# Optimization experiments

Hardware: AMD Instinct MI355X
Metric: run time of the kernel (lower is better)

The kernel has to match this reference:

```python
import jax, jax.numpy as jnp
import numpy as np

N_STRING = 6
N_SCALAR = 20
D_MODEL = 256
TOP_K = 4
LN_EPS = 1e-5


def setup_inputs() -> dict:
    key = jax.random.key(0)
    ks = jax.random.split(key, 16)
    B, d = 32768, D_MODEL
    s = 0.02
    inp = {
        "string_strategy_encodings": jax.random.normal(ks[0], (B, N_STRING, d), jnp.float32),
        "scalar_strategy_encodings": jax.random.normal(ks[1], (B, N_SCALAR, d), jnp.float32),
        "pair_scores": jax.random.normal(ks[2], (N_STRING, N_SCALAR), jnp.float32) * 0.1,
        "score_temperature": jnp.asarray(1.0, jnp.float32),
        # cross_modal_mlp: Linear(3d, d) -> ReLU -> Linear(d, d)
        "cm_w1": jax.random.normal(ks[3], (3 * d, d), jnp.float32) * s,
        "cm_b1": jnp.zeros((d,), jnp.float32),
        "cm_w2": jax.random.normal(ks[4], (d, d), jnp.float32) * s,
        "cm_b2": jnp.zeros((d,), jnp.float32),
        # diff_mlp: Linear(2d, d) -> ReLU -> Linear(d, d)
        "df_w1": jax.random.normal(ks[5], (2 * d, d), jnp.float32) * s,
        "df_b1": jnp.zeros((d,), jnp.float32),
        "df_w2": jax.random.normal(ks[6], (d, d), jnp.float32) * s,
        "df_b2": jnp.zeros((d,), jnp.float32),
        # fusion_mlp: Linear(3d, 2d) -> ReLU -> Linear(2d, d)
        "fu_w1": jax.random.normal(ks[7], (3 * d, 2 * d), jnp.float32) * s,
        "fu_b1": jnp.zeros((2 * d,), jnp.float32),
        "fu_w2": jax.random.normal(ks[8], (2 * d, d), jnp.float32) * s,
        "fu_b2": jnp.zeros((d,), jnp.float32),
        # output LayerNorm
        "ln_g": jnp.ones((d,), jnp.float32),
        "ln_b": jnp.zeros((d,), jnp.float32),
    }
    return inp


def _layernorm(x, g, b):
    mu = jnp.mean(x, axis=-1, keepdims=True)
    var = jnp.mean(jnp.square(x - mu), axis=-1, keepdims=True)
    return (x - mu) * jax.lax.rsqrt(var + LN_EPS) * g + b


def reference(string_strategy_encodings, scalar_strategy_encodings, pair_scores,
              score_temperature, cm_w1, cm_b1, cm_w2, cm_b2,
              df_w1, df_b1, df_w2, df_b2, fu_w1, fu_b1, fu_w2, fu_b2, ln_g, ln_b):
    n_string = string_strategy_encodings.shape[1]
    scores = pair_scores[:n_string, :]  # (6, 20); no masks (None path)
    flat = scores.reshape(-1)
    topk_vals, topk_idx = jax.lax.top_k(flat, TOP_K)
    ti = topk_idx // N_SCALAR  # string strategy indices (K,)
    tj = topk_idx % N_SCALAR   # scalar strategy indices (K,)
    temp = jnp.maximum(score_temperature, 0.1)
    weights = jax.nn.softmax(topk_vals / temp)  # (K,)

    s = jnp.take(string_strategy_encodings, ti, axis=1)  # (B, K, d)
    c = jnp.take(scalar_strategy_encodings, tj, axis=1)  # (B, K, d)
    prod = s * c

    cross_in = jnp.concatenate([s, c, prod], axis=-1)  # (B, K, 3d)
    cross_f = jax.nn.relu(cross_in @ cm_w1 + cm_b1) @ cm_w2 + cm_b2

    diff = s - c
    diff_in = jnp.concatenate([diff, jnp.abs(diff)], axis=-1)  # (B, K, 2d)
    diff_f = jax.nn.relu(diff_in @ df_w1 + df_b1) @ df_w2 + df_b2

    combined = jnp.concatenate([cross_f, diff_f, prod], axis=-1)  # (B, K, 3d)
    fused = jax.nn.relu(combined @ fu_w1 + fu_b1) @ fu_w2 + fu_b2
    rel = _layernorm(fused, ln_g, ln_b)  # (B, K, d)

    return jnp.einsum('k,bkd->bd', weights, rel)
```

## Files before the change

### kernel.cpp

```cpp
#include <hip/hip_runtime.h>
#include <stdint.h>


typedef __attribute__((ext_vector_type(8))) short frag8;
typedef __attribute__((ext_vector_type(4))) float f4;
typedef __attribute__((ext_vector_type(4))) int   i4;

#define MFMA16(a,b,c) __builtin_amdgcn_mfma_f32_16x16x32_bf16((a),(b),(c),0,0,0)

__device__ __forceinline__ short f2bf(float x) {
  unsigned u = __float_as_uint(x);
  return (short)((u + 0x7FFFu + ((u >> 16) & 1u)) >> 16);
}
__device__ __forceinline__ float bf2f(short s) {
  return __uint_as_float(((unsigned)(unsigned short)s) << 16);
}
__device__ __forceinline__ frag8 ldg8(const short* __restrict__ p) {
  return *reinterpret_cast<const frag8*>(p);
}


__global__ __launch_bounds__(256) void k_prep(
    const float* __restrict__ ps, const float* __restrict__ tempp,
    const float* __restrict__ w1, const float* __restrict__ w2,
    const float* __restrict__ dw1, const float* __restrict__ dw2,
    const float* __restrict__ fw1, const float* __restrict__ fw2,
    short* __restrict__ w1p, short* __restrict__ w2p,
    short* __restrict__ dw1p, short* __restrict__ dw2p,
    short* __restrict__ fw1p, short* __restrict__ fw2p,
    float* __restrict__ hdrf, int* __restrict__ hdri)
{
  if (blockIdx.x == 0) {
    const int lane = threadIdx.x;
    if (lane < 64) {
      const float NEG = -3.4e38f;
      float v0 = (lane < 120)      ? ps[lane]      : NEG;
      float v1 = (lane + 64 < 120) ? ps[lane + 64] : NEG;
      const int i0 = lane, i1 = lane + 64;
      unsigned elim = 0;
      float tv[4]; int bi[4];
      #pragma unroll
      for (int t = 0; t < 4; ++t) {
        float c0 = (elim & 1u) ? NEG : v0;
        float c1 = (elim & 2u) ? NEG : v1;
        float cv; int ci;
        if (c1 > c0) { cv = c1; ci = i1; } else { cv = c0; ci = i0; }
        #pragma unroll
        for (int off = 32; off >= 1; off >>= 1) {
          float ov = __shfl_xor(cv, off, 64);
          int   oi = __shfl_xor(ci, off, 64);
          if (ov > cv || (ov == cv && oi < ci)) { cv = ov; ci = oi; }
        }
        tv[t] = cv; bi[t] = ci;
        if (ci == i0) elim |= 1u;
        if (ci == i1) elim |= 2u;
      }
      if (lane == 0) {
        float tmp = fmaxf(tempp[0], 0.1f);
        float mx = tv[0];
        float e[4], s = 0.f;
        #pragma unroll
        for (int t = 0; t < 4; ++t) { e[t] = __expf((tv[t] - mx) / tmp); s += e[t]; }
        #pragma unroll
        for (int t = 0; t < 4; ++t) {
          hdrf[t]     = e[t] / s;
          hdri[4 + t] = bi[t] / 20;
          hdri[8 + t] = bi[t] % 20;
        }
      }
    }
    return;
  }
  int u = (blockIdx.x - 1) * 256 + threadIdx.x;
  const float* W; short* O; int N, KK;
  if      (u < 24576) {             W = w1;  O = w1p;  N = 256; KK = 24; }
  else if (u < 32768) { u -= 24576; W = w2;  O = w2p;  N = 256; KK = 8;  }
  else if (u < 49152) { u -= 32768; W = dw1; O = dw1p; N = 256; KK = 16; }
  else if (u < 57344) { u -= 49152; W = dw2; O = dw2p; N = 256; KK = 8;  }
  else if (u < 106496){ u -= 57344; W = fw1; O = fw1p; N = 512; KK = 24; }
  else                { u -= 106496;W = fw2; O = fw2p; N = 256; KK = 16; }
  int lane = u & 63, rest = u >> 6;
  int kk = rest % KK, ct = rest / KK;
  int k0 = kk * 32 + (lane >> 4) * 8;
  int n  = ct * 16 + (lane & 15);
  frag8 f;
  #pragma unroll
  for (int j = 0; j < 8; ++j) f[j] = f2bf(W[(size_t)(k0 + j) * N + n]);
  *reinterpret_cast<frag8*>(O + (size_t)u * 8) = f;
}

__global__ __launch_bounds__(256) void k_gather(
    const float* __restrict__ sEnc, const float* __restrict__ cEnc,
    const int* __restrict__ hdri,
    short* __restrict__ sg, short* __restrict__ cg, short* __restrict__ pg)
{
  int g = blockIdx.x * 256 + threadIdx.x;
  int lane = g & 63, rest = g >> 6;
  int kk = rest & 7, t16 = rest >> 3;
  int p = t16 * 16 + (lane & 15);
  int b = p >> 2, slot = p & 3;
  int k0 = kk * 32 + (lane >> 4) * 8;
  int ti = hdri[4 + slot], tj = hdri[8 + slot];
  const float* sp = sEnc + ((size_t)b * 6  + ti) * 256 + k0;
  const float* cp = cEnc + ((size_t)b * 20 + tj) * 256 + k0;
  f4 sA = *(const f4*)sp;  f4 sB = *(const f4*)(sp + 4);
  f4 cA = *(const f4*)cp;  f4 cB = *(const f4*)(cp + 4);
  frag8 fs, fc, fp;
  #pragma unroll
  for (int j = 0; j < 8; ++j) {
    float sv = (j < 4) ? sA[j] : sB[j - 4];
    float cv = (j < 4) ? cA[j] : cB[j - 4];
    fs[j] = f2bf(sv); fc[j] = f2bf(cv); fp[j] = f2bf(sv * cv);
  }
  size_t off = (size_t)g * 8;
  *reinterpret_cast<frag8*>(sg + off) = fs;
  *reinterpret_cast<frag8*>(cg + off) = fc;
  *reinterpret_cast<frag8*>(pg + off) = fp;
}

__device__ __forceinline__ void epi4(const f4 (&acc)[2][4],
                                     const float* __restrict__ bias, bool relu,
                                     short* __restrict__ dst, int stride,
                                     int wv, int m15, int q)
{
  #pragma unroll
  for (int c = 0; c < 4; ++c) {
    int col = wv * 64 + c * 16 + m15;
    float bv = bias[col];
    #pragma unroll
    for (int t = 0; t < 2; ++t) {
      #pragma unroll
      for (int r = 0; r < 4; ++r) {
        float x = acc[t][c][r] + bv;
        if (relu) x = fmaxf(x, 0.f);
        dst[(t * 16 + q * 4 + r) * stride + col] = f2bf(x);
      }
    }
  }
}

__global__ __launch_bounds__(256, 2) void k_main(
    const short* __restrict__ sg, const short* __restrict__ cg,
    const short* __restrict__ pg,
    const short* __restrict__ w1p,  const short* __restrict__ w2p,
    const short* __restrict__ dw1p, const short* __restrict__ dw2p,
    const short* __restrict__ fw1p, const short* __restrict__ fw2p,
    const float* __restrict__ cm_b1, const float* __restrict__ cm_b2,
    const float* __restrict__ df_b1, const float* __restrict__ df_b2,
    const float* __restrict__ fu_b1, const float* __restrict__ fu_b2,
    const float* __restrict__ ln_g,  const float* __restrict__ ln_b,
    const float* __restrict__ hdrf,  float* __restrict__ out)
{
  __shared__ short sCF[32 * 256];
  __shared__ short sDF[32 * 256];
  __shared__ short sXY[32 * 512];

  const int tid  = threadIdx.x;
  const int wv   = tid >> 6;
  const int lane = tid & 63;
  const int m15  = lane & 15;
  const int q    = lane >> 4;
  const int blk  = blockIdx.x;
  const int t0   = blk * 2, t1 = blk * 2 + 1;
  const f4 fz = {0.f, 0.f, 0.f, 0.f};

  {
    f4 acc[2][4];
    #pragma unroll
    for (int t = 0; t < 2; ++t) {
      #pragma unroll
      for (int c = 0; c < 4; ++c) acc[t][c] = fz;
    }
    auto seg = [&](const short* __restrict__ A, int kb) {
      #pragma unroll
      for (int kk = 0; kk < 8; ++kk) {
        frag8 a0 = ldg8(A + ((size_t)(t0 * 8 + kk) * 64 + lane) * 8);
        frag8 a1 = ldg8(A + ((size_t)(t1 * 8 + kk) * 64 + lane) * 8);
        #pragma unroll
        for (int c = 0; c < 4; ++c) {
          frag8 b = ldg8(w1p + ((size_t)((wv * 4 + c) * 24 + kb + kk) * 64 + lane) * 8);
          acc[0][c] = MFMA16(a0, b, acc[0][c]);
          acc[1][c] = MFMA16(a1, b, acc[1][c]);
        }
      }
    };
    seg(sg, 0); seg(cg, 8); seg(pg, 16);
    epi4(acc, cm_b1, true, sXY, 256, wv, m15, q);
  }
  __syncthreads();

  {
    f4 acc[2][4];
    #pragma unroll
    for (int t = 0; t < 2; ++t) {
      #pragma unroll
      for (int c = 0; c < 4; ++c) acc[t][c] = fz;
    }
    #pragma unroll
    for (int kk = 0; kk < 8; ++kk) {
      frag8 a0 = *reinterpret_cast<const frag8*>(&sXY[(m15) * 256 + kk * 32 + q * 8]);
      frag8 a1 = *reinterpret_cast<const frag8*>(&sXY[(16 + m15) * 256 + kk * 32 + q * 8]);
      #pragma unroll
      for (int c = 0; c < 4; ++c) {
        frag8 b = ldg8(w2p + ((size_t)((wv * 4 + c) * 8 + kk) * 64 + lane) * 8);
        acc[0][c] = MFMA16(a0, b, acc[0][c]);
        acc[1][c] = MFMA16(a1, b, acc[1][c]);
      }
    }
    epi4(acc, cm_b2, false, sCF, 256, wv, m15, q);
  }
  __syncthreads();

  {
    f4 acc[2][4];
    #pragma unroll
    for (int t = 0; t < 2; ++t) {
      #pragma unroll
      for (int c = 0; c < 4; ++c) acc[t][c] = fz;
    }
    #pragma unroll
    for (int kk = 0; kk < 8; ++kk) {
      frag8 s0 = ldg8(sg + ((size_t)(t0 * 8 + kk) * 64 + lane) * 8);
      frag8 s1 = ldg8(sg + ((size_t)(t1 * 8 + kk) * 64 + lane) * 8);
      frag8 c0 = ldg8(cg + ((size_t)(t0 * 8 + kk) * 64 + lane) * 8);
      frag8 c1 = ldg8(cg + ((size_t)(t1 * 8 + kk) * 64 + lane) * 8);
      frag8 d0, d1;
      #pragma unroll
      for (int j = 0; j < 8; ++j) {
        d0[j] = f2bf(bf2f(s0[j]) - bf2f(c0[j]));
        d1[j] = f2bf(bf2f(s1[j]) - bf2f(c1[j]));
      }
      i4 ai0 = __builtin_bit_cast(i4, d0);
      i4 ai1 = __builtin_bit_cast(i4, d1);
      #pragma unroll
      for (int jj = 0; jj < 4; ++jj) { ai0[jj] &= 0x7FFF7FFF; ai1[jj] &= 0x7FFF7FFF; }
      frag8 e0 = __builtin_bit_cast(frag8, ai0);
      frag8 e1 = __builtin_bit_cast(frag8, ai1);
      #pragma unroll
      for (int c = 0; c < 4; ++c) {
        frag8 b0 = ldg8(dw1p + ((size_t)((wv * 4 + c) * 16 + kk) * 64 + lane) * 8);
        acc[0][c] = MFMA16(d0, b0, acc[0][c]);
        acc[1][c] = MFMA16(d1, b0, acc[1][c]);
        frag8 b1 = ldg8(dw1p + ((size_t)((wv * 4 + c) * 16 + 8 + kk) * 64 + lane) * 8);
        acc[0][c] = MFMA16(e0, b1, acc[0][c]);
        acc[1][c] = MFMA16(e1, b1, acc[1][c]);
      }
    }
    epi4(acc, df_b1, true, sXY, 256, wv, m15, q);
  }
  __syncthreads();

  {
    f4 acc[2][4];
    #pragma unroll
    for (int t = 0; t < 2; ++t) {
      #pragma unroll
      for (int c = 0; c < 4; ++c) acc[t][c] = fz;
    }
    #pragma unroll
    for (int kk = 0; kk < 8; ++kk) {
      frag8 a0 = *reinterpret_cast<const frag8*>(&sXY[(m15) * 256 + kk * 32 + q * 8]);
      frag8 a1 = *reinterpret_cast<const frag8*>(&sXY[(16 + m15) * 256 + kk * 32 + q * 8]);
      #pragma unroll
      for (int c = 0; c < 4; ++c) {
        frag8 b = ldg8(dw2p + ((size_t)((wv * 4 + c) * 8 + kk) * 64 + lane) * 8);
        acc[0][c] = MFMA16(a0, b, acc[0][c]);
        acc[1][c] = MFMA16(a1, b, acc[1][c]);
      }
    }
    epi4(acc, df_b2, false, sDF, 256, wv, m15, q);
  }
  __syncthreads();

  {
    f4 acc[2][8];
    #pragma unroll
    for (int t = 0; t < 2; ++t) {
      #pragma unroll
      for (int c = 0; c < 8; ++c) acc[t][c] = fz;
    }
    auto segL = [&](const short* __restrict__ Abuf, int kb) {
      #pragma unroll
      for (int kk = 0; kk < 8; ++kk) {
        frag8 a0 = *reinterpret_cast<const frag8*>(&Abuf[(m15) * 256 + kk * 32 + q * 8]);
        frag8 a1 = *reinterpret_cast<const frag8*>(&Abuf[(16 + m15) * 256 + kk * 32 + q * 8]);
        #pragma unroll
        for (int c = 0; c < 8; ++c) {
          frag8 b = ldg8(fw1p + ((size_t)((wv * 8 + c) * 24 + kb + kk) * 64 + lane) * 8);
          acc[0][c] = MFMA16(a0, b, acc[0][c]);
          acc[1][c] = MFMA16(a1, b, acc[1][c]);
        }
      }
    };
    segL(sCF, 0); segL(sDF, 8);
    #pragma unroll
    for (int kk = 0; kk < 8; ++kk) {
      frag8 a0 = ldg8(pg + ((size_t)(t0 * 8 + kk) * 64 + lane) * 8);
      frag8 a1 = ldg8(pg + ((size_t)(t1 * 8 + kk) * 64 + lane) * 8);
      #pragma unroll
      for (int c = 0; c < 8; ++c) {
        frag8 b = ldg8(fw1p + ((size_t)((wv * 8 + c) * 24 + 16 + kk) * 64 + lane) * 8);
        acc[0][c] = MFMA16(a0, b, acc[0][c]);
        acc[1][c] = MFMA16(a1, b, acc[1][c]);
      }
    }
    #pragma unroll
    for (int c = 0; c < 8; ++c) {
      int col = wv * 128 + c * 16 + m15;
      float bv = fu_b1[col];
      #pragma unroll
      for (int t = 0; t < 2; ++t) {
        #pragma unroll
        for (int r = 0; r < 4; ++r) {
          float x = fmaxf(acc[t][c][r] + bv, 0.f);
          sXY[(t * 16 + q * 4 + r) * 512 + col] = f2bf(x);
        }
      }
    }
  }
  __syncthreads();

  {
    f4 acc[2][4];
    #pragma unroll
    for (int t = 0; t < 2; ++t) {
      #pragma unroll
      for (int c = 0; c < 4; ++c) acc[t][c] = fz;
    }
    #pragma unroll
    for (int kk = 0; kk < 16; ++kk) {
      frag8 a0 = *reinterpret_cast<const frag8*>(&sXY[(m15) * 512 + kk * 32 + q * 8]);
      frag8 a1 = *reinterpret_cast<const frag8*>(&sXY[(16 + m15) * 512 + kk * 32 + q * 8]);
      #pragma unroll
      for (int c = 0; c < 4; ++c) {
        frag8 b = ldg8(fw2p + ((size_t)((wv * 4 + c) * 16 + kk) * 64 + lane) * 8);
        acc[0][c] = MFMA16(a0, b, acc[0][c]);
        acc[1][c] = MFMA16(a1, b, acc[1][c]);
      }
    }
    float vals[2][4][4];
    #pragma unroll
    for (int c = 0; c < 4; ++c) {
      int col = wv * 64 + c * 16 + m15;
      float bv = fu_b2[col];
      #pragma unroll
      for (int t = 0; t < 2; ++t) {
        #pragma unroll
        for (int r = 0; r < 4; ++r) vals[t][c][r] = acc[t][c][r] + bv;
      }
    }
    float s1v[2][4], s2v[2][4];
    #pragma unroll
    for (int t = 0; t < 2; ++t) {
      #pragma unroll
      for (int r = 0; r < 4; ++r) {
        float a = 0.f, b = 0.f;
        #pragma unroll
        for (int c = 0; c < 4; ++c) { float v = vals[t][c][r]; a += v; b += v * v; }
        s1v[t][r] = a; s2v[t][r] = b;
      }
    }
    #pragma unroll
    for (int off = 8; off >= 1; off >>= 1) {
      #pragma unroll
      for (int t = 0; t < 2; ++t) {
        #pragma unroll
        for (int r = 0; r < 4; ++r) {
          s1v[t][r] += __shfl_xor(s1v[t][r], off, 64);
          s2v[t][r] += __shfl_xor(s2v[t][r], off, 64);
        }
      }
    }
    float* red = reinterpret_cast<float*>(sCF);
    if (m15 == 0) {
      #pragma unroll
      for (int t = 0; t < 2; ++t) {
        #pragma unroll
        for (int r = 0; r < 4; ++r) {
          int row = t * 16 + q * 4 + r;
          red[(row * 4 + wv) * 2 + 0] = s1v[t][r];
          red[(row * 4 + wv) * 2 + 1] = s2v[t][r];
        }
      }
    }
    __syncthreads();
    float mu[2][4], rs[2][4];
    #pragma unroll
    for (int t = 0; t < 2; ++t) {
      #pragma unroll
      for (int r = 0; r < 4; ++r) {
        int row = t * 16 + q * 4 + r;
        float S1 = 0.f, S2 = 0.f;
        #pragma unroll
        for (int w = 0; w < 4; ++w) {
          S1 += red[(row * 4 + w) * 2];
          S2 += red[(row * 4 + w) * 2 + 1];
        }
        float m_ = S1 * (1.0f / 256.0f);
        float v_ = S2 * (1.0f / 256.0f) - m_ * m_;
        mu[t][r] = m_;
        rs[t][r] = rsqrtf(v_ + 1e-5f);
      }
    }
    float wts[4] = {hdrf[0], hdrf[1], hdrf[2], hdrf[3]};
    #pragma unroll
    for (int c = 0; c < 4; ++c) {
      int col = wv * 64 + c * 16 + m15;
      float gv = ln_g[col], bv = ln_b[col];
      #pragma unroll
      for (int t = 0; t < 2; ++t) {
        float o = 0.f;
        #pragma unroll
        for (int r = 0; r < 4; ++r) {
          float rel = (vals[t][c][r] - mu[t][r]) * rs[t][r] * gv + bv;
          o += wts[r] * rel;
        }
        out[((size_t)(blk * 8 + t * 4 + q)) * 256 + col] = o;
      }
    }
  }
}

extern "C" void kernel_launch(void* const* d_in, const int* in_sizes, int n_in,
                              void* d_out, int out_size, void* d_ws, size_t ws_size,
                              hipStream_t stream)
{
  (void)in_sizes; (void)n_in; (void)out_size; (void)ws_size;
  const float* sEnc  = (const float*)d_in[0];
  const float* cEnc  = (const float*)d_in[1];
  const float* ps    = (const float*)d_in[2];
  const float* temp  = (const float*)d_in[3];
  const float* cm_w1 = (const float*)d_in[4];
  const float* cm_b1 = (const float*)d_in[5];
  const float* cm_w2 = (const float*)d_in[6];
  const float* cm_b2 = (const float*)d_in[7];
  const float* df_w1 = (const float*)d_in[8];
  const float* df_b1 = (const float*)d_in[9];
  const float* df_w2 = (const float*)d_in[10];
  const float* df_b2 = (const float*)d_in[11];
  const float* fu_w1 = (const float*)d_in[12];
  const float* fu_b1 = (const float*)d_in[13];
  const float* fu_w2 = (const float*)d_in[14];
  const float* fu_b2 = (const float*)d_in[15];
  const float* ln_g  = (const float*)d_in[16];
  const float* ln_b  = (const float*)d_in[17];

  char*  ws   = (char*)d_ws;
  float* hdrf = (float*)ws;
  int*   hdri = (int*)ws;
  short* w1p  = (short*)(ws + 256);
  short* w2p  = (short*)(ws + 393472);
  short* dw1p = (short*)(ws + 524544);
  short* dw2p = (short*)(ws + 786688);
  short* fw1p = (short*)(ws + 917760);
  short* fw2p = (short*)(ws + 1704192);
  short* sg   = (short*)(ws + 2097152);
  short* cg   = sg + (size_t)33554432;
  short* pg   = cg + (size_t)33554432;
  float* out  = (float*)d_out;

  k_prep<<<481, 256, 0, stream>>>(ps, temp, cm_w1, cm_w2, df_w1, df_w2, fu_w1, fu_w2,
                                  w1p, w2p, dw1p, dw2p, fw1p, fw2p, hdrf, hdri);
  k_gather<<<16384, 256, 0, stream>>>(sEnc, cEnc, (const int*)ws, sg, cg, pg);
  k_main<<<4096, 256, 0, stream>>>(sg, cg, pg, w1p, w2p, dw1p, dw2p, fw1p, fw2p,
                                   cm_b1, cm_b2, df_b1, df_b2, fu_b1, fu_b2,
                                   ln_g, ln_b, hdrf, out);
}
```

Baseline: 1.482 ms.

## Fuse gather into main kernel with 64-row tiles and fragment-layout LDS staging

Drops the separate gather kernel and its bf16 global intermediates (s, c, prod). The main kernel now loads the selected encodings straight from fp32 inputs into LDS in MFMA fragment layout. Each block of 512 threads handles 64 rows instead of 32, so every weight fragment loaded from global memory is reused over four row tiles. All intermediates live in a 128KB LDS arena with region reuse. This removes a large global write/read round trip and halves weight traffic per row, but the heavy LDS use likely limits occupancy to one block per CU.

```diff
diff --git a/kernel.cpp b/kernel.cpp
--- a/kernel.cpp
+++ b/kernel.cpp
@@ -89,59 +89,10 @@
   *reinterpret_cast<frag8*>(O + (size_t)u * 8) = f;
 }
 
-__global__ __launch_bounds__(256) void k_gather(
+
+__global__ __launch_bounds__(512, 2) void k_main(
     const float* __restrict__ sEnc, const float* __restrict__ cEnc,
-    const int* __restrict__ hdri,
-    short* __restrict__ sg, short* __restrict__ cg, short* __restrict__ pg)
-{
-  int g = blockIdx.x * 256 + threadIdx.x;
-  int lane = g & 63, rest = g >> 6;
-  int kk = rest & 7, t16 = rest >> 3;
-  int p = t16 * 16 + (lane & 15);
-  int b = p >> 2, slot = p & 3;
-  int k0 = kk * 32 + (lane >> 4) * 8;
-  int ti = hdri[4 + slot], tj = hdri[8 + slot];
-  const float* sp = sEnc + ((size_t)b * 6  + ti) * 256 + k0;
-  const float* cp = cEnc + ((size_t)b * 20 + tj) * 256 + k0;
-  f4 sA = *(const f4*)sp;  f4 sB = *(const f4*)(sp + 4);
-  f4 cA = *(const f4*)cp;  f4 cB = *(const f4*)(cp + 4);
-  frag8 fs, fc, fp;
-  #pragma unroll
-  for (int j = 0; j < 8; ++j) {
-    float sv = (j < 4) ? sA[j] : sB[j - 4];
-    float cv = (j < 4) ? cA[j] : cB[j - 4];
-    fs[j] = f2bf(sv); fc[j] = f2bf(cv); fp[j] = f2bf(sv * cv);
-  }
-  size_t off = (size_t)g * 8;
-  *reinterpret_cast<frag8*>(sg + off) = fs;
-  *reinterpret_cast<frag8*>(cg + off) = fc;
-  *reinterpret_cast<frag8*>(pg + off) = fp;
-}
-
-__device__ __forceinline__ void epi4(const f4 (&acc)[2][4],
-                                     const float* __restrict__ bias, bool relu,
-                                     short* __restrict__ dst, int stride,
-                                     int wv, int m15, int q)
-{
-  #pragma unroll
-  for (int c = 0; c < 4; ++c) {
-    int col = wv * 64 + c * 16 + m15;
-    float bv = bias[col];
-    #pragma unroll
-    for (int t = 0; t < 2; ++t) {
-      #pragma unroll
-      for (int r = 0; r < 4; ++r) {
-        float x = acc[t][c][r] + bv;
-        if (relu) x = fmaxf(x, 0.f);
-        dst[(t * 16 + q * 4 + r) * stride + col] = f2bf(x);
-      }
-    }
-  }
-}
-
-__global__ __launch_bounds__(256, 2) void k_main(
-    const short* __restrict__ sg, const short* __restrict__ cg,
-    const short* __restrict__ pg,
+    const int* __restrict__ hdri,  const float* __restrict__ hdrf,
     const short* __restrict__ w1p,  const short* __restrict__ w2p,
     const short* __restrict__ dw1p, const short* __restrict__ dw2p,
     const short* __restrict__ fw1p, const short* __restrict__ fw2p,
@@ -149,11 +100,13 @@
     const float* __restrict__ df_b1, const float* __restrict__ df_b2,
     const float* __restrict__ fu_b1, const float* __restrict__ fu_b2,
     const float* __restrict__ ln_g,  const float* __restrict__ ln_b,
-    const float* __restrict__ hdrf,  float* __restrict__ out)
+    float* __restrict__ out)
 {
-  __shared__ short sCF[32 * 256];
-  __shared__ short sDF[32 * 256];
-  __shared__ short sXY[32 * 512];
+  __shared__ __align__(16) short lds[65536];
+  short* R0 = lds;
+  short* R1 = lds + 16384;
+  short* R2 = lds + 32768;
+  short* R3 = lds + 49152;
 
   const int tid  = threadIdx.x;
   const int wv   = tid >> 6;
@@ -161,209 +114,260 @@
   const int m15  = lane & 15;
   const int q    = lane >> 4;
   const int blk  = blockIdx.x;
-  const int t0   = blk * 2, t1 = blk * 2 + 1;
+  const int row0 = blk * 64;
   const f4 fz = {0.f, 0.f, 0.f, 0.f};
 
   {
-    f4 acc[2][4];
-    #pragma unroll
-    for (int t = 0; t < 2; ++t) {
+    const int slot = m15 & 3;
+    const int ti = hdri[4 + slot], tj = hdri[8 + slot];
+    const int k0 = wv * 32 + q * 8;
+    #pragma unroll
+    for (int i = 0; i < 4; ++i) {
+      int row = row0 + i * 16 + m15;
+      int b = row >> 2;
+      const float* sp = sEnc + ((size_t)b * 6  + ti) * 256 + k0;
+      const float* cp = cEnc + ((size_t)b * 20 + tj) * 256 + k0;
+      f4 sA = *(const f4*)sp, sB = *(const f4*)(sp + 4);
+      f4 cA = *(const f4*)cp, cB = *(const f4*)(cp + 4);
+      frag8 fs, fc, fp;
+      #pragma unroll
+      for (int j = 0; j < 8; ++j) {
+        float sv = (j < 4) ? sA[j] : sB[j - 4];
+        float cv = (j < 4) ? cA[j] : cB[j - 4];
+        fs[j] = f2bf(sv); fc[j] = f2bf(cv); fp[j] = f2bf(sv * cv);
+      }
+      int off = ((i * 8 + wv) * 64 + lane) * 8;
+      *reinterpret_cast<frag8*>(R2 + off) = fs;
+      *reinterpret_cast<frag8*>(R0 + off) = fc;
+      *reinterpret_cast<frag8*>(R3 + off) = fp;
+    }
+  }
+  __syncthreads();
+
+  auto epiN256 = [&](const f4 (&acc)[4][2], const float* __restrict__ bias,
+                     bool relu, short* __restrict__ dst) {
+    #pragma unroll
+    for (int c = 0; c < 2; ++c) {
+      int col = wv * 32 + c * 16 + m15;
+      float bv = bias[col];
+      int kkf = col >> 5;
+      int lnq = (col >> 3) & 3;
+      int j   = col & 7;
+      #pragma unroll
+      for (int t = 0; t < 4; ++t) {
+        #pragma unroll
+        for (int r = 0; r < 4; ++r) {
+          float x = acc[t][c][r] + bv;
+          if (relu) x = fmaxf(x, 0.f);
+          dst[((t * 8 + kkf) * 64 + lnq * 16 + q * 4 + r) * 8 + j] = f2bf(x);
+        }
+      }
+    }
+  };
+
+  {
+    f4 acc[4][2];
+    #pragma unroll
+    for (int t = 0; t < 4; ++t) { acc[t][0] = fz; acc[t][1] = fz; }
+    #pragma unroll
+    for (int kk = 0; kk < 8; ++kk) {
+      frag8 as[4], ac[4], ap[4];
+      #pragma unroll
+      for (int t = 0; t < 4; ++t) {
+        int off = ((t * 8 + kk) * 64 + lane) * 8;
+        as[t] = *reinterpret_cast<const frag8*>(R2 + off);
+        ac[t] = *reinterpret_cast<const frag8*>(R0 + off);
+        ap[t] = *reinterpret_cast<const frag8*>(R3 + off);
+      }
+      #pragma unroll
+      for (int c = 0; c < 2; ++c) {
+        int ct = wv * 2 + c;
+        frag8 b0 = ldg8(w1p + ((size_t)(ct * 24 +      kk) * 64 + lane) * 8);
+        frag8 b1 = ldg8(w1p + ((size_t)(ct * 24 +  8 + kk) * 64 + lane) * 8);
+        frag8 b2 = ldg8(w1p + ((size_t)(ct * 24 + 16 + kk) * 64 + lane) * 8);
+        #pragma unroll
+        for (int t = 0; t < 4; ++t) {
+          acc[t][c] = MFMA16(as[t], b0, acc[t][c]);
+          acc[t][c] = MFMA16(ac[t], b1, acc[t][c]);
+          acc[t][c] = MFMA16(ap[t], b2, acc[t][c]);
+        }
+      }
+    }
+    epiN256(acc, cm_b1, true, R1);
+  }
+
+  {
+    f4 acc[4][2];
+    #pragma unroll
+    for (int t = 0; t < 4; ++t) { acc[t][0] = fz; acc[t][1] = fz; }
+    #pragma unroll
+    for (int kk = 0; kk < 8; ++kk) {
+      frag8 dfr[4], efr[4];
+      #pragma unroll
+      for (int t = 0; t < 4; ++t) {
+        int off = ((t * 8 + kk) * 64 + lane) * 8;
+        frag8 s = *reinterpret_cast<const frag8*>(R2 + off);
+        frag8 c = *reinterpret_cast<const frag8*>(R0 + off);
+        frag8 d;
+        #pragma unroll
+        for (int j = 0; j < 8; ++j) d[j] = f2bf(bf2f(s[j]) - bf2f(c[j]));
+        i4 ai = __builtin_bit_cast(i4, d);
+        #pragma unroll
+        for (int jj = 0; jj < 4; ++jj) ai[jj] &= 0x7FFF7FFF;
+        dfr[t] = d;
+        efr[t] = __builtin_bit_cast(frag8, ai);
+      }
+      #pragma unroll
+      for (int c = 0; c < 2; ++c) {
+        int ct = wv * 2 + c;
+        frag8 bd = ldg8(dw1p + ((size_t)(ct * 16 +     kk) * 64 + lane) * 8);
+        frag8 be = ldg8(dw1p + ((size_t)(ct * 16 + 8 + kk) * 64 + lane) * 8);
+        #pragma unroll
+        for (int t = 0; t < 4; ++t) {
+          acc[t][c] = MFMA16(dfr[t], bd, acc[t][c]);
+          acc[t][c] = MFMA16(efr[t], be, acc[t][c]);
+        }
+      }
+    }
+    __syncthreads();
+    epiN256(acc, df_b1, true, R2);
+    __syncthreads();
+  }
+
+  {
+    f4 acc[4][2];
+    #pragma unroll
+    for (int t = 0; t < 4; ++t) { acc[t][0] = fz; acc[t][1] = fz; }
+    #pragma unroll
+    for (int kk = 0; kk < 8; ++kk) {
+      frag8 a[4];
+      #pragma unroll
+      for (int t = 0; t < 4; ++t)
+        a[t] = *reinterpret_cast<const frag8*>(R1 + ((t * 8 + kk) * 64 + lane) * 8);
+      #pragma unroll
+      for (int c = 0; c < 2; ++c) {
+        frag8 b = ldg8(w2p + ((size_t)((wv * 2 + c) * 8 + kk) * 64 + lane) * 8);
+        #pragma unroll
+        for (int t = 0; t < 4; ++t) acc[t][c] = MFMA16(a[t], b, acc[t][c]);
+      }
+    }
+    epiN256(acc, cm_b2, false, R0);
+  }
+
+  {
+    f4 acc[4][2];
+    #pragma unroll
+    for (int t = 0; t < 4; ++t) { acc[t][0] = fz; acc[t][1] = fz; }
+    #pragma unroll
+    for (int kk = 0; kk < 8; ++kk) {
+      frag8 a[4];
+      #pragma unroll
+      for (int t = 0; t < 4; ++t)
+        a[t] = *reinterpret_cast<const frag8*>(R2 + ((t * 8 + kk) * 64 + lane) * 8);
+      #pragma unroll
+      for (int c = 0; c < 2; ++c) {
+        frag8 b = ldg8(dw2p + ((size_t)((wv * 2 + c) * 8 + kk) * 64 + lane) * 8);
+        #pragma unroll
+        for (int t = 0; t < 4; ++t) acc[t][c] = MFMA16(a[t], b, acc[t][c]);
+      }
+    }
+    __syncthreads();
+    epiN256(acc, df_b2, false, R1);
+    __syncthreads();
+  }
+
+  {
+    f4 acc[4][4];
+    #pragma unroll
+    for (int t = 0; t < 4; ++t)
       #pragma unroll
       for (int c = 0; c < 4; ++c) acc[t][c] = fz;
-    }
-    auto seg = [&](const short* __restrict__ A, int kb) {
-      #pragma unroll
-      for (int kk = 0; kk < 8; ++kk) {
-        frag8 a0 = ldg8(A + ((size_t)(t0 * 8 + kk) * 64 + lane) * 8);
-        frag8 a1 = ldg8(A + ((size_t)(t1 * 8 + kk) * 64 + lane) * 8);
-        #pragma unroll
-        for (int c = 0; c < 4; ++c) {
-          frag8 b = ldg8(w1p + ((size_t)((wv * 4 + c) * 24 + kb + kk) * 64 + lane) * 8);
-          acc[0][c] = MFMA16(a0, b, acc[0][c]);
-          acc[1][c] = MFMA16(a1, b, acc[1][c]);
-        }
-      }
-    };
-    seg(sg, 0); seg(cg, 8); seg(pg, 16);
-    epi4(acc, cm_b1, true, sXY, 256, wv, m15, q);
-  }
-  __syncthreads();
-
-  {
-    f4 acc[2][4];
-    #pragma unroll
-    for (int t = 0; t < 2; ++t) {
-      #pragma unroll
-      for (int c = 0; c < 4; ++c) acc[t][c] = fz;
-    }
     #pragma unroll
     for (int kk = 0; kk < 8; ++kk) {
-      frag8 a0 = *reinterpret_cast<const frag8*>(&sXY[(m15) * 256 + kk * 32 + q * 8]);
-      frag8 a1 = *reinterpret_cast<const frag8*>(&sXY[(16 + m15) * 256 + kk * 32 + q * 8]);
+      frag8 aF[4], aD[4], aP[4];
+      #pragma unroll
+      for (int t = 0; t < 4; ++t) {
+        int off = ((t * 8 + kk) * 64 + lane) * 8;
+        aF[t] = *reinterpret_cast<const frag8*>(R0 + off);
+        aD[t] = *reinterpret_cast<const frag8*>(R1 + off);
+        aP[t] = *reinterpret_cast<const frag8*>(R3 + off);
+      }
       #pragma unroll
       for (int c = 0; c < 4; ++c) {
-        frag8 b = ldg8(w2p + ((size_t)((wv * 4 + c) * 8 + kk) * 64 + lane) * 8);
-        acc[0][c] = MFMA16(a0, b, acc[0][c]);
-        acc[1][c] = MFMA16(a1, b, acc[1][c]);
-      }
-    }
-    epi4(acc, cm_b2, false, sCF, 256, wv, m15, q);
-  }
-  __syncthreads();
-
-  {
-    f4 acc[2][4];
-    #pragma unroll
-    for (int t = 0; t < 2; ++t) {
-      #pragma unroll
-      for (int c = 0; c < 4; ++c) acc[t][c] = fz;
-    }
-    #pragma unroll
-    for (int kk = 0; kk < 8; ++kk) {
-      frag8 s0 = ldg8(sg + ((size_t)(t0 * 8 + kk) * 64 + lane) * 8);
-      frag8 s1 = ldg8(sg + ((size_t)(t1 * 8 + kk) * 64 + lane) * 8);
-      frag8 c0 = ldg8(cg + ((size_t)(t0 * 8 + kk) * 64 + lane) * 8);
-      frag8 c1 = ldg8(cg + ((size_t)(t1 * 8 + kk) * 64 + lane) * 8);
-      frag8 d0, d1;
-      #pragma unroll
-      for (int j = 0; j < 8; ++j) {
-        d0[j] = f2bf(bf2f(s0[j]) - bf2f(c0[j]));
-        d1[j] = f2bf(bf2f(s1[j]) - bf2f(c1[j]));
-      }
-      i4 ai0 = __builtin_bit_cast(i4, d0);
-      i4 ai1 = __builtin_bit_cast(i4, d1);
-      #pragma unroll
-      for (int jj = 0; jj < 4; ++jj) { ai0[jj] &= 0x7FFF7FFF; ai1[jj] &= 0x7FFF7FFF; }
-      frag8 e0 = __builtin_bit_cast(frag8, ai0);
-      frag8 e1 = __builtin_bit_cast(frag8, ai1);
-      #pragma unroll
-      for (int c = 0; c < 4; ++c) {
-        frag8 b0 = ldg8(dw1p + ((size_t)((wv * 4 + c) * 16 + kk) * 64 + lane) * 8);
-        acc[0][c] = MFMA16(d0, b0, acc[0][c]);
-        acc[1][c] = MFMA16(d1, b0, acc[1][c]);
-        frag8 b1 = ldg8(dw1p + ((size_t)((wv * 4 + c) * 16 + 8 + kk) * 64 + lane) * 8);
-        acc[0][c] = MFMA16(e0, b1, acc[0][c]);
-        acc[1][c] = MFMA16(e1, b1, acc[1][c]);
-      }
-    }
-    epi4(acc, df_b1, true, sXY, 256, wv, m15, q);
-  }
-  __syncthreads();
-
-  {
-    f4 acc[2][4];
-    #pragma unroll
-    for (int t = 0; t < 2; ++t) {
-      #pragma unroll
-      for (int c = 0; c < 4; ++c) acc[t][c] = fz;
-    }
-    #pragma unroll
-    for (int kk = 0; kk < 8; ++kk) {
-      frag8 a0 = *reinterpret_cast<const frag8*>(&sXY[(m15) * 256 + kk * 32 + q * 8]);
-      frag8 a1 = *reinterpret_cast<const frag8*>(&sXY[(16 + m15) * 256 + kk * 32 + q * 8]);
-      #pragma unroll
-      for (int c = 0; c < 4; ++c) {
-        frag8 b = ldg8(dw2p + ((size_t)((wv * 4 + c) * 8 + kk) * 64 + lane) * 8);
-        acc[0][c] = MFMA16(a0, b, acc[0][c]);
-        acc[1][c] = MFMA16(a1, b, acc[1][c]);
-      }
-    }
-    epi4(acc, df_b2, false, sDF, 256, wv, m15, q);
-  }
-  __syncthreads();
-
-  {
-    f4 acc[2][8];
-    #pragma unroll
-    for (int t = 0; t < 2; ++t) {
-      #pragma unroll
-      for (int c = 0; c < 8; ++c) acc[t][c] = fz;
-    }
-    auto segL = [&](const short* __restrict__ Abuf, int kb) {
-      #pragma unroll
-      for (int kk = 0; kk < 8; ++kk) {
-        frag8 a0 = *reinterpret_cast<const frag8*>(&Abuf[(m15) * 256 + kk * 32 + q * 8]);
-        frag8 a1 = *reinterpret_cast<const frag8*>(&Abuf[(16 + m15) * 256 + kk * 32 + q * 8]);
-        #pragma unroll
-        for (int c = 0; c < 8; ++c) {
-          frag8 b = ldg8(fw1p + ((size_t)((wv * 8 + c) * 24 + kb + kk) * 64 + lane) * 8);
-          acc[0][c] = MFMA16(a0, b, acc[0][c]);
-          acc[1][c] = MFMA16(a1, b, acc[1][c]);
-        }
-      }
-    };
-    segL(sCF, 0); segL(sDF, 8);
-    #pragma unroll
-    for (int kk = 0; kk < 8; ++kk) {
-      frag8 a0 = ldg8(pg + ((size_t)(t0 * 8 + kk) * 64 + lane) * 8);
-      frag8 a1 = ldg8(pg + ((size_t)(t1 * 8 + kk) * 64 + lane) * 8);
-      #pragma unroll
-      for (int c = 0; c < 8; ++c) {
-        frag8 b = ldg8(fw1p + ((size_t)((wv * 8 + c) * 24 + 16 + kk) * 64 + lane) * 8);
-        acc[0][c] = MFMA16(a0, b, acc[0][c]);
-        acc[1][c] = MFMA16(a1, b, acc[1][c]);
-      }
-    }
-    #pragma unroll
-    for (int c = 0; c < 8; ++c) {
-      int col = wv * 128 + c * 16 + m15;
+        int ct = wv * 4 + c;
+        frag8 b0 = ldg8(fw1p + ((size_t)(ct * 24 +      kk) * 64 + lane) * 8);
+        frag8 b1 = ldg8(fw1p + ((size_t)(ct * 24 +  8 + kk) * 64 + lane) * 8);
+        frag8 b2 = ldg8(fw1p + ((size_t)(ct * 24 + 16 + kk) * 64 + lane) * 8);
+        #pragma unroll
+        for (int t = 0; t < 4; ++t) {
+          acc[t][c] = MFMA16(aF[t], b0, acc[t][c]);
+          acc[t][c] = MFMA16(aD[t], b1, acc[t][c]);
+          acc[t][c] = MFMA16(aP[t], b2, acc[t][c]);
+        }
+      }
+    }
+    __syncthreads();
+    #pragma unroll
+    for (int c = 0; c < 4; ++c) {
+      int col = wv * 64 + c * 16 + m15;
       float bv = fu_b1[col];
-      #pragma unroll
-      for (int t = 0; t < 2; ++t) {
+      int kkf = col >> 5;
+      int lnq = (col >> 3) & 3;
+      int j   = col & 7;
+      #pragma unroll
+      for (int t = 0; t < 4; ++t) {
         #pragma unroll
         for (int r = 0; r < 4; ++r) {
           float x = fmaxf(acc[t][c][r] + bv, 0.f);
-          sXY[(t * 16 + q * 4 + r) * 512 + col] = f2bf(x);
-        }
-      }
-    }
-  }
-  __syncthreads();
-
-  {
-    f4 acc[2][4];
-    #pragma unroll
-    for (int t = 0; t < 2; ++t) {
-      #pragma unroll
-      for (int c = 0; c < 4; ++c) acc[t][c] = fz;
-    }
+          R2[((t * 16 + kkf) * 64 + lnq * 16 + q * 4 + r) * 8 + j] = f2bf(x);
+        }
+      }
+    }
+    __syncthreads();
+  }
+
+  {
+    f4 acc[4][2];
+    #pragma unroll
+    for (int t = 0; t < 4; ++t) { acc[t][0] = fz; acc[t][1] = fz; }
     #pragma unroll
     for (int kk = 0; kk < 16; ++kk) {
-      frag8 a0 = *reinterpret_cast<const frag8*>(&sXY[(m15) * 512 + kk * 32 + q * 8]);
-      frag8 a1 = *reinterpret_cast<const frag8*>(&sXY[(16 + m15) * 512 + kk * 32 + q * 8]);
-      #pragma unroll
-      for (int c = 0; c < 4; ++c) {
-        frag8 b = ldg8(fw2p + ((size_t)((wv * 4 + c) * 16 + kk) * 64 + lane) * 8);
-        acc[0][c] = MFMA16(a0, b, acc[0][c]);
-        acc[1][c] = MFMA16(a1, b, acc[1][c]);
-      }
-    }
-    float vals[2][4][4];
-    #pragma unroll
-    for (int c = 0; c < 4; ++c) {
-      int col = wv * 64 + c * 16 + m15;
+      frag8 a[4];
+      #pragma unroll
+      for (int t = 0; t < 4; ++t)
+        a[t] = *reinterpret_cast<const frag8*>(R2 + ((t * 16 + kk) * 64 + lane) * 8);
+      #pragma unroll
+      for (int c = 0; c < 2; ++c) {
+        frag8 b = ldg8(fw2p + ((size_t)((wv * 2 + c) * 16 + kk) * 64 + lane) * 8);
+        #pragma unroll
+        for (int t = 0; t < 4; ++t) acc[t][c] = MFMA16(a[t], b, acc[t][c]);
+      }
+    }
+    float vals[4][2][4];
+    #pragma unroll
+    for (int c = 0; c < 2; ++c) {
+      int col = wv * 32 + c * 16 + m15;
       float bv = fu_b2[col];
       #pragma unroll
-      for (int t = 0; t < 2; ++t) {
+      for (int t = 0; t < 4; ++t)
         #pragma unroll
         for (int r = 0; r < 4; ++r) vals[t][c][r] = acc[t][c][r] + bv;
-      }
-    }
-    float s1v[2][4], s2v[2][4];
-    #pragma unroll
-    for (int t = 0; t < 2; ++t) {
+    }
+    float s1v[4][4], s2v[4][4];
+    #pragma unroll
+    for (int t = 0; t < 4; ++t) {
       #pragma unroll
       for (int r = 0; r < 4; ++r) {
         float a = 0.f, b = 0.f;
         #pragma unroll
-        for (int c = 0; c < 4; ++c) { float v = vals[t][c][r]; a += v; b += v * v; }
+        for (int c = 0; c < 2; ++c) { float v = vals[t][c][r]; a += v; b += v * v; }
         s1v[t][r] = a; s2v[t][r] = b;
       }
     }
     #pragma unroll
     for (int off = 8; off >= 1; off >>= 1) {
       #pragma unroll
-      for (int t = 0; t < 2; ++t) {
+      for (int t = 0; t < 4; ++t) {
         #pragma unroll
         for (int r = 0; r < 4; ++r) {
           s1v[t][r] += __shfl_xor(s1v[t][r], off, 64);
@@ -371,30 +375,30 @@
         }
       }
     }
-    float* red = reinterpret_cast<float*>(sCF);
+    float* red = reinterpret_cast<float*>(R0);
     if (m15 == 0) {
       #pragma unroll
-      for (int t = 0; t < 2; ++t) {
+      for (int t = 0; t < 4; ++t) {
         #pragma unroll
         for (int r = 0; r < 4; ++r) {
           int row = t * 16 + q * 4 + r;
-          red[(row * 4 + wv) * 2 + 0] = s1v[t][r];
-          red[(row * 4 + wv) * 2 + 1] = s2v[t][r];
-        }
-      }
-    }
-    __syncthreads();
-    float mu[2][4], rs[2][4];
-    #pragma unroll
-    for (int t = 0; t < 2; ++t) {
+          red[(row * 8 + wv) * 2 + 0] = s1v[t][r];
+          red[(row * 8 + wv) * 2 + 1] = s2v[t][r];
+        }
+      }
+    }
+    __syncthreads();
+    float mu[4][4], rs[4][4];
+    #pragma unroll
+    for (int t = 0; t < 4; ++t) {
       #pragma unroll
       for (int r = 0; r < 4; ++r) {
         int row = t * 16 + q * 4 + r;
         float S1 = 0.f, S2 = 0.f;
         #pragma unroll
-        for (int w = 0; w < 4; ++w) {
-          S1 += red[(row * 4 + w) * 2];
-          S2 += red[(row * 4 + w) * 2 + 1];
+        for (int w = 0; w < 8; ++w) {
+          S1 += red[(row * 8 + w) * 2];
+          S2 += red[(row * 8 + w) * 2 + 1];
         }
         float m_ = S1 * (1.0f / 256.0f);
         float v_ = S2 * (1.0f / 256.0f) - m_ * m_;
@@ -404,18 +408,18 @@
     }
     float wts[4] = {hdrf[0], hdrf[1], hdrf[2], hdrf[3]};
     #pragma unroll
-    for (int c = 0; c < 4; ++c) {
-      int col = wv * 64 + c * 16 + m15;
+    for (int c = 0; c < 2; ++c) {
+      int col = wv * 32 + c * 16 + m15;
       float gv = ln_g[col], bv = ln_b[col];
       #pragma unroll
-      for (int t = 0; t < 2; ++t) {
+      for (int t = 0; t < 4; ++t) {
         float o = 0.f;
         #pragma unroll
         for (int r = 0; r < 4; ++r) {
           float rel = (vals[t][c][r] - mu[t][r]) * rs[t][r] * gv + bv;
           o += wts[r] * rel;
         }
-        out[((size_t)(blk * 8 + t * 4 + q)) * 256 + col] = o;
+        out[((size_t)(blk * 16 + t * 4 + q)) * 256 + col] = o;
       }
     }
   }
@@ -454,15 +458,12 @@
   short* dw2p = (short*)(ws + 786688);
   short* fw1p = (short*)(ws + 917760);
   short* fw2p = (short*)(ws + 1704192);
-  short* sg   = (short*)(ws + 2097152);
-  short* cg   = sg + (size_t)33554432;
-  short* pg   = cg + (size_t)33554432;
   float* out  = (float*)d_out;
 
   k_prep<<<481, 256, 0, stream>>>(ps, temp, cm_w1, cm_w2, df_w1, df_w2, fu_w1, fu_w2,
                                   w1p, w2p, dw1p, dw2p, fw1p, fw2p, hdrf, hdri);
-  k_gather<<<16384, 256, 0, stream>>>(sEnc, cEnc, (const int*)ws, sg, cg, pg);
-  k_main<<<4096, 256, 0, stream>>>(sg, cg, pg, w1p, w2p, dw1p, dw2p, fw1p, fw2p,
+  k_main<<<2048, 512, 0, stream>>>(sEnc, cEnc, hdri, hdrf,
+                                   w1p, w2p, dw1p, dw2p, fw1p, fw2p,
                                    cm_b1, cm_b2, df_b1, df_b2, fu_b1, fu_b2,
-                                   ln_g, ln_b, hdrf, out);
-}
+                                   ln_g, ln_b, out);
+}
```

Result: faster. 1.321 ms (-10.9%).
